# Optimization experiments

Hardware: AMD Instinct MI355X
Metric: run time of the kernel (lower is better)

Reference implementation:

```python
import jax, jax.numpy as jnp
import numpy as np

EPS = 1e-5
NEG_SLOPE = 0.2


def _batched_dynamic_conv(x, kernels):
    # x: [B, C, H, W]; kernels: [B, Cout, Cin, 3, 3]. Per-sample distinct
    # kernels == one grouped conv with feature_group_count = B.
    B, C, H, W = x.shape
    Cout = kernels.shape[1]
    xg = x.reshape(1, B * C, H, W)
    kg = kernels.reshape(B * Cout, C, 3, 3)
    y = jax.lax.conv_general_dilated(
        xg, kg, window_strides=(1, 1), padding=((1, 1), (1, 1)),
        feature_group_count=B,
        dimension_numbers=('NCHW', 'OIHW', 'NCHW'))
    return y.reshape(B, Cout, H, W)


def _instance_norm(y):
    # InstanceNorm2d(affine=False): per (b, c) over spatial dims, biased var.
    mean = jnp.mean(y, axis=(2, 3), keepdims=True)
    var = jnp.var(y, axis=(2, 3), keepdims=True)
    return (y - mean) * jax.lax.rsqrt(var + EPS)


def _leaky_relu(y):
    return jnp.where(y >= 0, y, NEG_SLOPE * y)


def setup_inputs() -> dict:
    key = jax.random.key(0)
    k1, k2, k3 = jax.random.split(key, 3)
    B, C, H, W = 16, 64, 128, 128
    x = jax.random.normal(k1, (B, C, H, W), dtype=jnp.float32)
    kernel1 = jax.random.normal(k2, (B, C, C, 3, 3), dtype=jnp.float32) * 0.05
    kernel2 = jax.random.normal(k3, (B, C, C, 3, 3), dtype=jnp.float32) * 0.05
    return {"x": x, "kernel1": kernel1, "kernel2": kernel2}


def reference(x, kernel1, kernel2):
    h = _leaky_relu(_instance_norm(_batched_dynamic_conv(x, kernel1)))
    h = _instance_norm(_batched_dynamic_conv(h, kernel2))
    return _leaky_relu(x + h)
```

## Files before the change

### kernel.cpp

```cpp
#include <hip/hip_runtime.h>
#include <stdint.h>
#include <stddef.h>

#define BATCH 16
#define CH    64
#define IH    128
#define IW    128
#define HW    (IH*IW)

#define PROW 8320
#define PB   1081600

typedef __attribute__((ext_vector_type(8))) short short8;
typedef __attribute__((ext_vector_type(4))) short short4v;
typedef __attribute__((ext_vector_type(4))) float f32x4;
typedef __attribute__((ext_vector_type(2))) float f32x2;

__device__ __forceinline__ float bf2f(short s) {
    union { unsigned int u; float f; } v;
    v.u = ((unsigned int)(unsigned short)s) << 16;
    return v.f;
}
__device__ __forceinline__ short f2bf(float f) {
    union { float f; unsigned int u; } v; v.f = f;
    unsigned int r = v.u + 0x7fffu + ((v.u >> 16) & 1u);
    return (short)(r >> 16);
}

__device__ __forceinline__ void gload_lds16(const short* g, short* l) {
    __builtin_amdgcn_global_load_lds(
        (const __attribute__((address_space(1))) void*)g,
        (__attribute__((address_space(3))) void*)l, 16, 0, 0);
}

__global__ __launch_bounds__(256) void prep_all(const float* __restrict__ x,
                                                const float* __restrict__ w1,
                                                const float* __restrict__ w2,
                                                short* __restrict__ xpad,
                                                short* __restrict__ hpad,
                                                short* __restrict__ w1t,
                                                short* __restrict__ w2t) {
    const int bid = blockIdx.x;
    const int t = threadIdx.x;
    if (bid < 2048) {
        __shared__ float tile[CH * 129];
        const int b = bid >> 7;
        const int y = bid & 127;
        const float* src = x + (size_t)b * CH * HW + (size_t)y * IW;
        #pragma unroll
        for (int i = 0; i < 32; ++i) {
            int lin = i * 256 + t;
            int c = lin >> 7, xx = lin & 127;
            tile[c * 129 + xx] = src[(size_t)c * HW + xx];
        }
        __syncthreads();
        unsigned int* dst = (unsigned int*)(xpad) + (size_t)b * (PB / 2) + (size_t)(y + 1) * (PROW / 2);
        #pragma unroll
        for (int j = 0; j < 16; ++j) {
            int lin = j * 256 + t;
            int c2 = lin & 31, xx = lin >> 5;
            unsigned int lo = (unsigned int)(unsigned short)f2bf(tile[(2 * c2) * 129 + xx]);
            unsigned int hi = (unsigned int)(unsigned short)f2bf(tile[(2 * c2 + 1) * 129 + xx]);
            dst[(c2 >> 4) * 2080 + (xx + 1) * 16 + (c2 & 15)] = lo | (hi << 16);
        }
    } else if (bid < 2560) {
        int b2 = bid - 2048;
        const float* src = w1; short* dst = w1t;
        if (b2 >= 256) { src = w2; dst = w2t; b2 -= 256; }
        int gt = b2 * 256 + t;
        int ci   = gt & 31;
        int cout = (gt >> 5) & 63;
        int cc   = (gt >> 11) & 1;
        int b    = gt >> 12;
        const float* s = src + ((size_t)(b * 64 + cout)) * 576 + (cc * 32 + ci) * 9;
        short* d = dst + ((size_t)(b * 2 + cc) * 9) * 2048 + cout * 32 + ci;
        #pragma unroll
        for (int tap = 0; tap < 9; ++tap)
            d[tap * 2048] = f2bf(s[tap]);
    } else {
        int b2 = bid - 2560;
        short* p = ((b2 & 1) ? hpad : xpad) + (size_t)(b2 >> 1) * PB;
        const short8 z = {0,0,0,0,0,0,0,0};
        #pragma unroll
        for (int i = 0; i < 17; ++i) {
            int s = i * 256 + t;
            if (s >= 4128) break;
            if (s < 2080) {
                int row = (s < 1040) ? 0 : 129;
                int o = (s < 1040 ? s : s - 1040) * 8;
                *(short8*)&p[(size_t)row * PROW + o] = z;
            } else {
                int u = s - 2080;
                int k = u & 3, col = (u >> 2) & 1, cc = (u >> 3) & 1, pr = (u >> 4) + 1;
                *(short8*)&p[(size_t)pr * PROW + cc * 4160 + (col ? 129 * 32 : 0) + k * 8] = z;
            }
        }
    }
}

__global__ __launch_bounds__(256, 2) void conv_kernel(
    const short* __restrict__ in, const short* __restrict__ wt,
    short* __restrict__ out,
    float* __restrict__ part_s, float* __restrict__ part_q) {

    __shared__ short act[4 * PROW];

    const int b    = blockIdx.y;
    const int t    = threadIdx.x;
    const int lane = t & 63;
    const int wave = t >> 6;
    const int l15  = lane & 15;
    const int q    = lane >> 4;
    const int ph   = wave & 1;
    const int wr   = wave >> 1;
    const int y0   = (blockIdx.x << 1) + wr;
    const int xb   = ph * 64;

    const short* inB = in + (size_t)b * PB;

    {
        const short* grow = inB + (size_t)((blockIdx.x << 1) + wave) * PROW;
        short* lrow = &act[wave * PROW];
        #pragma unroll
        for (int i = 0; i < 16; ++i)
            gload_lds16(grow + i * 512 + lane * 8, lrow + i * 512);
        if (lane < 16)
            gload_lds16(grow + 16 * 512 + lane * 8, lrow + 16 * 512);
    }
    __syncthreads();

    const short* wgl = wt + (size_t)b * 36864;
    const int aoff = l15 * 32 + q * 8;
    const int boff = (xb + l15) * 32 + q * 8;

    const f32x4 zero4 = {0.f, 0.f, 0.f, 0.f};
    f32x4 acc[4][4];
    #pragma unroll
    for (int mi = 0; mi < 4; ++mi)
        #pragma unroll
        for (int ni = 0; ni < 4; ++ni) acc[mi][ni] = zero4;

    #pragma unroll
    for (int cc = 0; cc < 2; ++cc) {
        #pragma unroll
        for (int tap = 0; tap < 9; ++tap) {
            const int dy = tap / 3, dx = tap % 3;
            const short* arow = wgl + (cc * 9 + tap) * 2048 + aoff;
            const int bbase = (wr + dy) * PROW + cc * 4160 + dx * 32 + boff;
            short8 a[4], bb[4];
            #pragma unroll
            for (int mi = 0; mi < 4; ++mi)
                a[mi] = *(const short8*)&arow[mi * 512];
            #pragma unroll
            for (int ni = 0; ni < 4; ++ni)
                bb[ni] = *(const short8*)&act[bbase + ni * 512];
            #pragma unroll
            for (int mi = 0; mi < 4; ++mi)
                #pragma unroll
                for (int ni = 0; ni < 4; ++ni)
                    acc[mi][ni] = __builtin_amdgcn_mfma_f32_16x16x32_bf16(
                        a[mi], bb[ni], acc[mi][ni], 0, 0, 0);
        }
    }

    const int pbase = ((b * 128 + y0) * 2 + ph) * 64;
    #pragma unroll
    for (int mi = 0; mi < 4; ++mi) {
        float psum[4] = {0.f,0.f,0.f,0.f};
        float psq[4]  = {0.f,0.f,0.f,0.f};
        #pragma unroll
        for (int ni = 0; ni < 4; ++ni) {
            int xx = xb + ni * 16 + l15;
            size_t base = (size_t)b * PB + (size_t)(1 + y0) * PROW
                          + (mi >> 1) * 4160 + (size_t)(1 + xx) * 32
                          + (mi & 1) * 16 + q * 4;
            short4v o;
            #pragma unroll
            for (int g = 0; g < 4; ++g) {
                float v = acc[mi][ni][g];
                o[g] = f2bf(v);
                psum[g] += v;
                psq[g]  += v * v;
            }
            *(short4v*)&out[base] = o;
        }
        #pragma unroll
        for (int g = 0; g < 4; ++g) {
            float s = psum[g], s2 = psq[g];
            #pragma unroll
            for (int off = 1; off < 16; off <<= 1) {
                s  += __shfl_xor(s,  off, 64);
                s2 += __shfl_xor(s2, off, 64);
            }
            if (l15 == 0) {
                int idx = pbase + mi * 16 + q * 4 + g;
                part_s[idx] = s;
                part_q[idx] = s2;
            }
        }
    }
}

__global__ __launch_bounds__(256) void finalize_stats(const float* __restrict__ part_s,
                                                      const float* __restrict__ part_q,
                                                      float* __restrict__ nrm) {
    __shared__ float red[2][4][64];
    const int b = blockIdx.x;
    const int c = threadIdx.x & 63;
    const int g = threadIdx.x >> 6;
    const float* ps = part_s + (size_t)b * 16384 + c;
    const float* pq = part_q + (size_t)b * 16384 + c;
    float s = 0.f, s2 = 0.f;
    #pragma unroll 8
    for (int r = 0; r < 64; ++r) {
        s  += ps[(g * 64 + r) * 64];
        s2 += pq[(g * 64 + r) * 64];
    }
    red[0][g][c] = s;
    red[1][g][c] = s2;
    __syncthreads();
    if (threadIdx.x < 64) {
        float S = red[0][0][c] + red[0][1][c] + red[0][2][c] + red[0][3][c];
        float Q = red[1][0][c] + red[1][1][c] + red[1][2][c] + red[1][3][c];
        const float inv = 1.0f / (float)HW;
        float mean = S * inv;
        float var = Q * inv - mean * mean;
        float scale = rsqrtf(var + 1e-5f);
        f32x2 sb = {scale, -mean * scale};
        ((f32x2*)nrm)[b * CH + c] = sb;
    }
}

__global__ __launch_bounds__(256) void norm_leaky(short* __restrict__ hpad,
                                                  const float* __restrict__ nrm) {
    const int bid = blockIdx.x;
    const int b = bid >> 7, y = bid & 127;
    short* row = hpad + (size_t)b * PB + (size_t)(y + 1) * PROW;
    const int t = threadIdx.x;
    #pragma unroll
    for (int i = 0; i < 4; ++i) {
        int s = i * 256 + t;
        int c8 = s & 3, xx = (s >> 2) & 127, cc = s >> 9;
        short* p = row + cc * 4160 + (xx + 1) * 32 + c8 * 8;
        const f32x2* nb = (const f32x2*)nrm + b * CH + cc * 32 + c8 * 8;
        short8 v = *(const short8*)p;
        short8 o;
        #pragma unroll
        for (int j = 0; j < 8; ++j) {
            f32x2 sb = nb[j];
            float f = sb.x * bf2f(v[j]) + sb.y;
            f = f >= 0.f ? f : 0.2f * f;
            o[j] = f2bf(f);
        }
        *(short8*)p = o;
    }
}

__global__ __launch_bounds__(256) void final_kernel(const float* __restrict__ x,
                                                    const short* __restrict__ y2,
                                                    const float* __restrict__ nrm,
                                                    float* __restrict__ out) {
    __shared__ float tile[64 * 65];
    const int x0 = blockIdx.x * 64;
    const int y  = blockIdx.y;
    const int b  = blockIdx.z;
    const int t  = threadIdx.x;
    const f32x2* nb = (const f32x2*)nrm + b * CH;
    const size_t rowb = (size_t)b * PB + (size_t)(y + 1) * PROW;
    #pragma unroll
    for (int i = 0; i < 2; ++i) {
        int s = i * 256 + t;
        int xx = s >> 3;
        int c0 = (s & 7) * 8;
        int cc = c0 >> 5, cl = c0 & 31;
        short8 v = *(const short8*)&y2[rowb + cc * 4160 + (size_t)(x0 + xx + 1) * 32 + cl];
        #pragma unroll
        for (int j = 0; j < 8; ++j) {
            f32x2 sb = nb[c0 + j];
            tile[(c0 + j) * 65 + xx] = sb.x * bf2f(v[j]) + sb.y;
        }
    }
    __syncthreads();
    #pragma unroll
    for (int i = 0; i < 4; ++i) {
        int lin = i * 1024 + t * 4;
        int c = lin >> 6;
        int xx = lin & 63;
        size_t g = ((size_t)(b * CH + c) * IH + y) * IW + x0 + xx;
        f32x4 xv = *(const f32x4*)&x[g];
        f32x4 o;
        #pragma unroll
        for (int k = 0; k < 4; ++k) {
            float f = xv[k] + tile[c * 65 + xx + k];
            o[k] = f >= 0.f ? f : 0.2f * f;
        }
        *(f32x4*)&out[g] = o;
    }
}

extern "C" void kernel_launch(void* const* d_in, const int* in_sizes, int n_in,
                              void* d_out, int out_size, void* d_ws, size_t ws_size,
                              hipStream_t stream) {
    const float* x  = (const float*)d_in[0];
    const float* w1 = (const float*)d_in[1];
    const float* w2 = (const float*)d_in[2];
    float* out = (float*)d_out;
    char* ws = (char*)d_ws;

    const size_t SZ_PAD  = 34611200ull;
    const size_t SZ_PART = 1048576ull;
    short* xpad = (short*)(ws);
    short* hpad = (short*)(ws + SZ_PAD);
    short* w1t  = (short*)(ws + 2 * SZ_PAD);
    short* w2t  = (short*)(ws + 2 * SZ_PAD + 1179648ull);
    float* ps1  = (float*)(ws + 2 * SZ_PAD + 2359296ull);
    float* pq1  = (float*)(ws + 2 * SZ_PAD + 2359296ull + SZ_PART);
    float* ps2  = (float*)(ws + 2 * SZ_PAD + 2359296ull + 2 * SZ_PART);
    float* pq2  = (float*)(ws + 2 * SZ_PAD + 2359296ull + 3 * SZ_PART);
    float* nrm1 = (float*)(ws + 2 * SZ_PAD + 2359296ull + 4 * SZ_PART);
    float* nrm2 = nrm1 + BATCH * CH * 2;

    if (ws_size < 2 * SZ_PAD + 2359296ull + 4 * SZ_PART + 8192) return;

    prep_all<<<2592, 256, 0, stream>>>(x, w1, w2, xpad, hpad, w1t, w2t);
    conv_kernel<<<dim3(64, 16), 256, 0, stream>>>(xpad, w1t, hpad, ps1, pq1);
    finalize_stats<<<16, 256, 0, stream>>>(ps1, pq1, nrm1);
    norm_leaky<<<2048, 256, 0, stream>>>(hpad, nrm1);
    conv_kernel<<<dim3(64, 16), 256, 0, stream>>>(hpad, w2t, xpad, ps2, pq2);
    finalize_stats<<<16, 256, 0, stream>>>(ps2, pq2, nrm2);
    final_kernel<<<dim3(2, 128, 16), 256, 0, stream>>>(x, xpad, nrm2, out);
}
```

Baseline: 239.2 us.

## Fuse instance-norm and leaky ReLU into second conv's activation load, retile conv

The separate norm_leaky pass is removed. The second conv now reads the raw conv1 output, applies the per-channel scale/shift and leaky ReLU while staging it into LDS, and zeroes the padding border in place, so hpad's border no longer has to be pre-zeroed. The conv block is retiled: each block now covers 4 output rows and one 64-column half using a smaller segmented LDS buffer, with occupancy raised to 3 blocks per CU. Weight fragments are double-buffered in registers across the taps. The fused path trades async global-to-LDS loads for register loads plus ALU work, and the tile now reloads halo rows more often.

```diff
diff --git a/kernel.cpp b/kernel.cpp
--- a/kernel.cpp
+++ b/kernel.cpp
@@ -10,6 +10,7 @@
 
 #define PROW 8320
 #define PB   1081600
+#define SEG  2112
 
 typedef __attribute__((ext_vector_type(8))) short short8;
 typedef __attribute__((ext_vector_type(4))) short short4v;
@@ -37,7 +38,6 @@
                                                 const float* __restrict__ w1,
                                                 const float* __restrict__ w2,
                                                 short* __restrict__ xpad,
-                                                short* __restrict__ hpad,
                                                 short* __restrict__ w1t,
                                                 short* __restrict__ w2t) {
     const int bid = blockIdx.x;
@@ -79,7 +79,7 @@
             d[tap * 2048] = f2bf(s[tap]);
     } else {
         int b2 = bid - 2560;
-        short* p = ((b2 & 1) ? hpad : xpad) + (size_t)(b2 >> 1) * PB;
+        short* p = xpad + (size_t)b2 * PB;
         const short8 z = {0,0,0,0,0,0,0,0};
         #pragma unroll
         for (int i = 0; i < 17; ++i) {
@@ -98,12 +98,13 @@
     }
 }
 
-__global__ __launch_bounds__(256, 2) void conv_kernel(
+template<bool FUSED>
+__global__ __launch_bounds__(256, 3) void conv_kernel(
     const short* __restrict__ in, const short* __restrict__ wt,
-    short* __restrict__ out,
+    short* __restrict__ out, const float* __restrict__ nrm,
     float* __restrict__ part_s, float* __restrict__ part_q) {
 
-    __shared__ short act[4 * PROW];
+    __shared__ short act[12 * SEG];
 
     const int b    = blockIdx.y;
     const int t    = threadIdx.x;
@@ -111,27 +112,70 @@
     const int wave = t >> 6;
     const int l15  = lane & 15;
     const int q    = lane >> 4;
-    const int ph   = wave & 1;
-    const int wr   = wave >> 1;
-    const int y0   = (blockIdx.x << 1) + wr;
-    const int xb   = ph * 64;
+    const int bx   = blockIdx.x >> 1;
+    const int ph2  = blockIdx.x & 1;
+    const int xp0  = ph2 * 64;
+    const int y0   = bx * 4 + wave;
 
     const short* inB = in + (size_t)b * PB;
-
-    {
-        const short* grow = inB + (size_t)((blockIdx.x << 1) + wave) * PROW;
-        short* lrow = &act[wave * PROW];
-        #pragma unroll
-        for (int i = 0; i < 16; ++i)
-            gload_lds16(grow + i * 512 + lane * 8, lrow + i * 512);
-        if (lane < 16)
-            gload_lds16(grow + 16 * 512 + lane * 8, lrow + 16 * 512);
-    }
-    __syncthreads();
-
     const short* wgl = wt + (size_t)b * 36864;
     const int aoff = l15 * 32 + q * 8;
-    const int boff = (xb + l15) * 32 + q * 8;
+
+    short8 a2[2][4];
+    #pragma unroll
+    for (int mi = 0; mi < 4; ++mi)
+        a2[0][mi] = *(const short8*)&wgl[aoff + mi * 512];
+
+    if (!FUSED) {
+        #pragma unroll
+        for (int k = 0; k < 3; ++k) {
+            const int s = wave + k * 4;
+            const int rg = bx * 4 + (s >> 1);
+            const short* gseg = inB + (size_t)rg * PROW + (s & 1) * 4160 + xp0 * 32;
+            short* lseg = &act[s * SEG];
+            #pragma unroll
+            for (int c = 0; c < 4; ++c)
+                gload_lds16(gseg + c * 512 + lane * 8, lseg + c * 512);
+            if (lane < 8)
+                gload_lds16(gseg + 2048 + lane * 8, lseg + 2048);
+        }
+    } else {
+        const int scc = wave & 1;
+        const int ci0 = (lane & 3) * 8;
+        f32x2 sb[8];
+        #pragma unroll
+        for (int j = 0; j < 8; ++j)
+            sb[j] = ((const f32x2*)nrm)[b * CH + scc * 32 + ci0 + j];
+        #pragma unroll
+        for (int k = 0; k < 3; ++k) {
+            const int s = wave + k * 4;
+            const int rg = bx * 4 + (s >> 1);
+            const bool rowpad = (rg == 0) || (rg == 129);
+            const short* gseg = inB + (size_t)rg * PROW + scc * 4160 + xp0 * 32;
+            short* lseg = &act[s * SEG];
+            #pragma unroll
+            for (int c = 0; c < 5; ++c) {
+                if (c < 4 || lane < 8) {
+                    short8 v = *(const short8*)&gseg[c * 512 + lane * 8];
+                    const int lpx = c * 16 + (lane >> 2);
+                    const bool xm = (ph2 == 0 && lpx == 0) || (ph2 == 1 && lpx == 65);
+                    short8 o;
+                    if (rowpad || xm) {
+                        o = (short8){0,0,0,0,0,0,0,0};
+                    } else {
+                        #pragma unroll
+                        for (int j = 0; j < 8; ++j) {
+                            float f = sb[j].x * bf2f(v[j]) + sb[j].y;
+                            f = f >= 0.f ? f : 0.2f * f;
+                            o[j] = f2bf(f);
+                        }
+                    }
+                    *(short8*)&lseg[c * 512 + lane * 8] = o;
+                }
+            }
+        }
+    }
+    __syncthreads();
 
     const f32x4 zero4 = {0.f, 0.f, 0.f, 0.f};
     f32x4 acc[4][4];
@@ -141,36 +185,36 @@
         for (int ni = 0; ni < 4; ++ni) acc[mi][ni] = zero4;
 
     #pragma unroll
-    for (int cc = 0; cc < 2; ++cc) {
-        #pragma unroll
-        for (int tap = 0; tap < 9; ++tap) {
-            const int dy = tap / 3, dx = tap % 3;
-            const short* arow = wgl + (cc * 9 + tap) * 2048 + aoff;
-            const int bbase = (wr + dy) * PROW + cc * 4160 + dx * 32 + boff;
-            short8 a[4], bb[4];
+    for (int s = 0; s < 18; ++s) {
+        const int cc = s / 9, tap = s % 9;
+        const int dy = tap / 3, dx = tap % 3;
+        if (s + 1 < 18) {
+            const short* anext = wgl + (s + 1) * 2048 + aoff;
             #pragma unroll
             for (int mi = 0; mi < 4; ++mi)
-                a[mi] = *(const short8*)&arow[mi * 512];
+                a2[(s + 1) & 1][mi] = *(const short8*)&anext[mi * 512];
+        }
+        const int segb = ((wave + dy) * 2 + cc) * SEG;
+        short8 bb[4];
+        #pragma unroll
+        for (int ni = 0; ni < 4; ++ni)
+            bb[ni] = *(const short8*)&act[segb + (dx + ni * 16 + l15) * 32 + q * 8];
+        #pragma unroll
+        for (int mi = 0; mi < 4; ++mi)
             #pragma unroll
             for (int ni = 0; ni < 4; ++ni)
-                bb[ni] = *(const short8*)&act[bbase + ni * 512];
-            #pragma unroll
-            for (int mi = 0; mi < 4; ++mi)
-                #pragma unroll
-                for (int ni = 0; ni < 4; ++ni)
-                    acc[mi][ni] = __builtin_amdgcn_mfma_f32_16x16x32_bf16(
-                        a[mi], bb[ni], acc[mi][ni], 0, 0, 0);
-        }
-    }
-
-    const int pbase = ((b * 128 + y0) * 2 + ph) * 64;
+                acc[mi][ni] = __builtin_amdgcn_mfma_f32_16x16x32_bf16(
+                    a2[s & 1][mi], bb[ni], acc[mi][ni], 0, 0, 0);
+    }
+
+    const int pbase = ((b * 128 + y0) * 2 + ph2) * 64;
     #pragma unroll
     for (int mi = 0; mi < 4; ++mi) {
         float psum[4] = {0.f,0.f,0.f,0.f};
         float psq[4]  = {0.f,0.f,0.f,0.f};
         #pragma unroll
         for (int ni = 0; ni < 4; ++ni) {
-            int xx = xb + ni * 16 + l15;
+            int xx = xp0 + ni * 16 + l15;
             size_t base = (size_t)b * PB + (size_t)(1 + y0) * PROW
                           + (mi >> 1) * 4160 + (size_t)(1 + xx) * 32
                           + (mi & 1) * 16 + q * 4;
@@ -231,31 +275,6 @@
     }
 }
 
-__global__ __launch_bounds__(256) void norm_leaky(short* __restrict__ hpad,
-                                                  const float* __restrict__ nrm) {
-    const int bid = blockIdx.x;
-    const int b = bid >> 7, y = bid & 127;
-    short* row = hpad + (size_t)b * PB + (size_t)(y + 1) * PROW;
-    const int t = threadIdx.x;
-    #pragma unroll
-    for (int i = 0; i < 4; ++i) {
-        int s = i * 256 + t;
-        int c8 = s & 3, xx = (s >> 2) & 127, cc = s >> 9;
-        short* p = row + cc * 4160 + (xx + 1) * 32 + c8 * 8;
-        const f32x2* nb = (const f32x2*)nrm + b * CH + cc * 32 + c8 * 8;
-        short8 v = *(const short8*)p;
-        short8 o;
-        #pragma unroll
-        for (int j = 0; j < 8; ++j) {
-            f32x2 sb = nb[j];
-            float f = sb.x * bf2f(v[j]) + sb.y;
-            f = f >= 0.f ? f : 0.2f * f;
-            o[j] = f2bf(f);
-        }
-        *(short8*)p = o;
-    }
-}
-
 __global__ __launch_bounds__(256) void final_kernel(const float* __restrict__ x,
                                                     const short* __restrict__ y2,
                                                     const float* __restrict__ nrm,
@@ -322,11 +341,10 @@
 
     if (ws_size < 2 * SZ_PAD + 2359296ull + 4 * SZ_PART + 8192) return;
 
-    prep_all<<<2592, 256, 0, stream>>>(x, w1, w2, xpad, hpad, w1t, w2t);
-    conv_kernel<<<dim3(64, 16), 256, 0, stream>>>(xpad, w1t, hpad, ps1, pq1);
+    prep_all<<<2576, 256, 0, stream>>>(x, w1, w2, xpad, w1t, w2t);
+    conv_kernel<false><<<dim3(64, 16), 256, 0, stream>>>(xpad, w1t, hpad, nullptr, ps1, pq1);
     finalize_stats<<<16, 256, 0, stream>>>(ps1, pq1, nrm1);
-    norm_leaky<<<2048, 256, 0, stream>>>(hpad, nrm1);
-    conv_kernel<<<dim3(64, 16), 256, 0, stream>>>(hpad, w2t, xpad, ps2, pq2);
+    conv_kernel<true><<<dim3(64, 16), 256, 0, stream>>>(hpad, w2t, xpad, nrm1, ps2, pq2);
     finalize_stats<<<16, 256, 0, stream>>>(ps2, pq2, nrm2);
     final_kernel<<<dim3(2, 128, 16), 256, 0, stream>>>(x, xpad, nrm2, out);
 }
```

Result: faster. 231.0 us (-3.4%).
